# Kernel tuning notes

Measured on AMD Instinct MI355X. Metric: run time of the kernel, lower is better.

## Reference

```python
import jax, jax.numpy as jnp
import numpy as np

HIDDEN = 768
HEADS = 8
EXP = 4
EPS = 1e-5


def layer_norm(x, g, b):
    mu = jnp.mean(x, axis=-1, keepdims=True)
    var = jnp.mean(jnp.square(x - mu), axis=-1, keepdims=True)
    return (x - mu) * jax.lax.rsqrt(var + EPS) * g + b


def setup_inputs() -> dict:
    key = jax.random.key(0)
    ks = jax.random.split(key, 16)
    h, e = HIDDEN, EXP * HIDDEN
    s = 0.02
    return {
        "x": jax.random.normal(ks[0], (2, 4096, h), dtype=jnp.float32),
        "ln1_g": jnp.ones((h,), jnp.float32),
        "ln1_b": jnp.zeros((h,), jnp.float32),
        "wq": jax.random.normal(ks[1], (h, h), jnp.float32) * s,
        "bq": jnp.zeros((h,), jnp.float32),
        "wk": jax.random.normal(ks[2], (h, h), jnp.float32) * s,
        "bk": jnp.zeros((h,), jnp.float32),
        "wv": jax.random.normal(ks[3], (h, h), jnp.float32) * s,
        "bv": jnp.zeros((h,), jnp.float32),
        "wp": jax.random.normal(ks[4], (h, h), jnp.float32) * s,
        "bp": jnp.zeros((h,), jnp.float32),
        "ln2_g": jnp.ones((h,), jnp.float32),
        "ln2_b": jnp.zeros((h,), jnp.float32),
        "w1": jax.random.normal(ks[5], (h, e), jnp.float32) * s,
        "b1": jnp.zeros((e,), jnp.float32),
        "w2": jax.random.normal(ks[6], (e, h), jnp.float32) * s,
        "b2": jnp.zeros((h,), jnp.float32),
    }


def reference(x, ln1_g, ln1_b, wq, bq, wk, bk, wv, bv, wp, bp,
              ln2_g, ln2_b, w1, b1, w2, b2):
    n, s, h = x.shape
    d = h // HEADS

    # --- MSA branch (pre-LN) ---
    xn = layer_norm(x, ln1_g, ln1_b)
    q = (xn @ wq + bq).reshape(n, s, HEADS, d).transpose(0, 2, 1, 3)  # bhsd
    k = (xn @ wk + bk).reshape(n, s, HEADS, d).transpose(0, 2, 1, 3)
    v = (xn @ wv + bv).reshape(n, s, HEADS, d).transpose(0, 2, 1, 3)
    energy = jnp.einsum('bhqd,bhkd->bhqk', q, k)
    # faithful to original: softmax over the HEAD axis (dim=1), then scale
    att = jax.nn.softmax(energy, axis=1) / (h ** 0.5)
    attn_out = jnp.einsum('bhqk,bhkd->bhqd', att, v)
    attn_out = attn_out.transpose(0, 2, 1, 3).reshape(n, s, h)
    attn_out = attn_out @ wp + bp
    x = x + attn_out

    # --- MLP branch (pre-LN) ---
    xn = layer_norm(x, ln2_g, ln2_b)
    hmid = jax.nn.gelu(xn @ w1 + b1, approximate=False)
    x = x + (hmid @ w2 + b2)
    return x
```

## Files before the change

### kernel.cpp

```cpp
#include <hip/hip_runtime.h>
#include <cstdint>
#include <cstddef>

#define AS1 __attribute__((address_space(1)))
#define AS3 __attribute__((address_space(3)))

typedef __attribute__((ext_vector_type(8))) __bf16 bf16x8;
typedef __attribute__((ext_vector_type(4))) float f32x4;

__device__ __forceinline__ void gload_lds16(const void* g, void* l) {
  __builtin_amdgcn_global_load_lds((AS1 void*)g, (AS3 void*)l, 16, 0, 0);
}

__global__ void k_transpose_w(const float* __restrict__ src, __bf16* __restrict__ dst,
                              int K, int N, int ldd, int koff) {
  __shared__ float tile[32][33];
  const int bx = blockIdx.x * 32;
  const int by = blockIdx.y * 32;
  const int tx = threadIdx.x, ty = threadIdx.y;
#pragma unroll
  for (int ii = 0; ii < 4; ++ii) {
    int i = ty + ii * 8;
    tile[i][tx] = src[(size_t)(by + i) * N + bx + tx];
  }
  __syncthreads();
#pragma unroll
  for (int ii = 0; ii < 4; ++ii) {
    int i = ty + ii * 8;
    dst[(size_t)(bx + i) * ldd + koff + by + tx] = (__bf16)tile[tx][i];
  }
}

__global__ void k_transpose_w4(const float* __restrict__ s0, const float* __restrict__ s1,
                               const float* __restrict__ s2, const float* __restrict__ s3,
                               __bf16* __restrict__ d0, __bf16* __restrict__ d1,
                               __bf16* __restrict__ d2, __bf16* __restrict__ d3) {
  __shared__ float tile[32][33];
  const float* src;
  __bf16* dst;
  switch (blockIdx.z) {
    case 0: src = s0; dst = d0; break;
    case 1: src = s1; dst = d1; break;
    case 2: src = s2; dst = d2; break;
    default: src = s3; dst = d3; break;
  }
  const int bx = blockIdx.x * 32, by = blockIdx.y * 32;
  const int tx = threadIdx.x, ty = threadIdx.y;
#pragma unroll
  for (int ii = 0; ii < 4; ++ii) {
    int i = ty + ii * 8;
    tile[i][tx] = src[(size_t)(by + i) * 768 + bx + tx];
  }
  __syncthreads();
#pragma unroll
  for (int ii = 0; ii < 4; ++ii) {
    int i = ty + ii * 8;
    dst[(size_t)(bx + i) * 768 + by + tx] = (__bf16)tile[tx][i];
  }
}

__global__ void k_pack_bias(const float* __restrict__ bq, const float* __restrict__ bk,
                            const float* __restrict__ bv, float* __restrict__ dst) {
  int i = blockIdx.x * 256 + threadIdx.x;
  if (i < 768) dst[i] = bq[i];
  else if (i < 1536) dst[i] = bk[i - 768];
  else if (i < 2304) dst[i] = bv[i - 1536];
}

__global__ __launch_bounds__(256) void k_layernorm(const float* __restrict__ x,
                                                   const float* __restrict__ g,
                                                   const float* __restrict__ b,
                                                   __bf16* __restrict__ out) {
  const int row = blockIdx.x * 4 + (threadIdx.x >> 6);
  const int lane = threadIdx.x & 63;
  const float* xr = x + (size_t)row * 768;
  float4 v[3];
#pragma unroll
  for (int j = 0; j < 3; ++j) v[j] = *(const float4*)(xr + j * 256 + lane * 4);
  float s = 0.f, ss = 0.f;
#pragma unroll
  for (int j = 0; j < 3; ++j) {
    s += v[j].x + v[j].y + v[j].z + v[j].w;
    ss += v[j].x * v[j].x + v[j].y * v[j].y + v[j].z * v[j].z + v[j].w * v[j].w;
  }
#pragma unroll
  for (int off = 32; off > 0; off >>= 1) {
    s += __shfl_xor(s, off);
    ss += __shfl_xor(ss, off);
  }
  const float mu = s * (1.f / 768.f);
  const float rstd = rsqrtf(ss * (1.f / 768.f) - mu * mu + 1e-5f);
  __bf16* orow = out + (size_t)row * 768;
#pragma unroll
  for (int j = 0; j < 3; ++j) {
    float4 gg = *(const float4*)(g + j * 256 + lane * 4);
    float4 bb = *(const float4*)(b + j * 256 + lane * 4);
    const int base = j * 256 + lane * 4;
    orow[base + 0] = (__bf16)((v[j].x - mu) * rstd * gg.x + bb.x);
    orow[base + 1] = (__bf16)((v[j].y - mu) * rstd * gg.y + bb.y);
    orow[base + 2] = (__bf16)((v[j].z - mu) * rstd * gg.z + bb.z);
    orow[base + 3] = (__bf16)((v[j].w - mu) * rstd * gg.w + bb.w);
  }
}

template <int MODE>
__global__ __launch_bounds__(256) void k_gemm(const __bf16* __restrict__ A,
                                              const __bf16* __restrict__ BT,
                                              const float* __restrict__ bias,
                                              const float* __restrict__ resid,
                                              void* __restrict__ Cout,
                                              int M, int N, int K, int lda, int ldb) {
  __shared__ __bf16 As[128 * 32];
  __shared__ __bf16 Bs[128 * 32];
  const int nx = N >> 7;
  const int rpx = (M >> 7) >> 3;
  const int xcd = blockIdx.x & 7;
  const int ib = blockIdx.x >> 3;
  const int n0 = (ib % nx) << 7;
  const int m0 = (xcd * rpx + ib / nx) << 7;
  if constexpr (MODE == 3) {
    A += (size_t)blockIdx.y * K;
    BT += (size_t)blockIdx.y * K;
  }
  const int tid = threadIdx.x;
  const int wid = tid >> 6, lane = tid & 63;
  const int wm = wid >> 1, wn = wid & 1;
  const int lr = lane & 15, lg = lane >> 4;

  f32x4 acc[4][4] = {};

  for (int k0 = 0; k0 < K; k0 += 32) {
#pragma unroll
    for (int it = 0; it < 2; ++it) {
      int t = tid + it * 256;
      int r = t >> 2, c = (t & 3) * 8;
      gload_lds16(A + (size_t)(m0 + r) * lda + k0 + c, As + t * 8);
      gload_lds16(BT + (size_t)(n0 + r) * ldb + k0 + c, Bs + t * 8);
    }
    __syncthreads();
    bf16x8 af[4], bf[4];
#pragma unroll
    for (int i = 0; i < 4; ++i) af[i] = *(const bf16x8*)(As + (wm * 64 + i * 16 + lr) * 32 + lg * 8);
#pragma unroll
    for (int j = 0; j < 4; ++j) bf[j] = *(const bf16x8*)(Bs + (wn * 64 + j * 16 + lr) * 32 + lg * 8);
#pragma unroll
    for (int i = 0; i < 4; ++i)
#pragma unroll
      for (int j = 0; j < 4; ++j)
        acc[i][j] = __builtin_amdgcn_mfma_f32_16x16x32_bf16(af[i], bf[j], acc[i][j], 0, 0, 0);
    __syncthreads();
  }

#pragma unroll
  for (int i = 0; i < 4; ++i)
#pragma unroll
    for (int j = 0; j < 4; ++j)
#pragma unroll
      for (int r = 0; r < 4; ++r) {
        int row = m0 + wm * 64 + i * 16 + lg * 4 + r;
        int col = n0 + wn * 64 + j * 16 + lr;
        float v = acc[i][j][r];
        if constexpr (MODE != 3) v += bias[col];
        size_t idx = (size_t)row * N + col;
        if constexpr (MODE == 0) {
          if (col < 768) v *= 1.44269504088896f;
          ((__bf16*)Cout)[idx] = (__bf16)v;
        } else if constexpr (MODE == 1) {
          ((float*)Cout)[idx] = v + resid[idx];
        } else if constexpr (MODE == 2) {
          float u = 0.7978845608f * (v + 0.044715f * v * v * v);
          float t = __builtin_amdgcn_exp2f(u * 2.88539008f);
          float th = 1.f - 2.f * __builtin_amdgcn_rcpf(t + 1.f);
          ((__bf16*)Cout)[idx] = (__bf16)(0.5f * v * (1.f + th));
        } else {
          ((__bf16*)Cout)[(size_t)blockIdx.y * M * N + idx] = (__bf16)v;
        }
      }
}

__global__ __launch_bounds__(256) void k_fuse_mlp2(const __bf16* __restrict__ p0,
                                                   const __bf16* __restrict__ p1,
                                                   const float* __restrict__ bias,
                                                   const float* __restrict__ resid,
                                                   float* __restrict__ out) {
  int g = blockIdx.x * 256 + threadIdx.x;
  int base = g * 8;
  int col = base % 768;
  bf16x8 a = *(const bf16x8*)(p0 + base);
  bf16x8 b = *(const bf16x8*)(p1 + base);
  float4 r0 = *(const float4*)(resid + base);
  float4 r1 = *(const float4*)(resid + base + 4);
  float4 b0 = *(const float4*)(bias + col);
  float4 b1 = *(const float4*)(bias + col + 4);
  float4 o0, o1;
  o0.x = r0.x + b0.x + (float)a[0] + (float)b[0];
  o0.y = r0.y + b0.y + (float)a[1] + (float)b[1];
  o0.z = r0.z + b0.z + (float)a[2] + (float)b[2];
  o0.w = r0.w + b0.w + (float)a[3] + (float)b[3];
  o1.x = r1.x + b1.x + (float)a[4] + (float)b[4];
  o1.y = r1.y + b1.y + (float)a[5] + (float)b[5];
  o1.z = r1.z + b1.z + (float)a[6] + (float)b[6];
  o1.w = r1.w + b1.w + (float)a[7] + (float)b[7];
  *(float4*)(out + base) = o0;
  *(float4*)(out + base + 4) = o1;
}

__global__ __launch_bounds__(256) void k_pack_kv(const __bf16* __restrict__ qkv,
                                                 __bf16* __restrict__ KA,
                                                 __bf16* __restrict__ VA) {
  __shared__ __bf16 vtile[32][772];
  const int g = blockIdx.x, b = blockIdx.y;
  const int t = threadIdx.x;
#pragma unroll
  for (int half = 0; half < 2; ++half) {
    int kb = g * 2 + half;
#pragma unroll
    for (int i = 0; i < 6; ++i) {
      int c = t + i * 256;
      int lane = c & 63, f = c >> 6;
      int dc = f % 3, hh = (f / 3) & 1, hp = f / 6;
      int row = kb * 16 + (lane & 15);
      int col = 768 + hp * 192 + hh * 96 + dc * 32 + (lane >> 4) * 8;
      bf16x8 v = *(const bf16x8*)(qkv + (size_t)(b * 4096 + row) * 2304 + col);
      *(bf16x8*)(KA + ((size_t)(b * 256 + kb) * 1536 + c) * 8) = v;
    }
  }
#pragma unroll
  for (int i = 0; i < 12; ++i) {
    int c = t + i * 256;
    int row = c / 96, c8 = c % 96;
    *(bf16x8*)(&vtile[row][c8 * 8]) =
        *(const bf16x8*)(qkv + (size_t)(b * 4096 + g * 32 + row) * 2304 + 1536 + c8 * 8);
  }
  __syncthreads();
#pragma unroll
  for (int i = 0; i < 12; ++i) {
    int c = t + i * 256;
    int lane = c & 63, f = c >> 6;
    int db = f % 6, hh = (f / 6) & 1, hp = f / 12;
    int d = hp * 192 + hh * 96 + db * 16 + (lane & 15);
    int lg_ = lane >> 4;
    bf16x8 v;
#pragma unroll
    for (int e = 0; e < 8; ++e) {
      int krow = (e >> 2) * 16 + lg_ * 4 + (e & 3);
      v[e] = vtile[krow][d];
    }
    *(bf16x8*)(VA + ((size_t)(b * 128 + g) * 3072 + c) * 8) = v;
  }
}

__global__ __launch_bounds__(1024, 4) void k_attn(const __bf16* __restrict__ qkv,
                                                  const __bf16* __restrict__ KA,
                                                  const __bf16* __restrict__ VA,
                                                  __bf16* __restrict__ attn2) {
  __shared__ __bf16 Kb_s[2][12288];
  __shared__ __bf16 Vb_s[24576];
  __shared__ float ps_s[2][4352];
  const int bid = blockIdx.x;
  const int slice = bid & 3;
  const int b = slice >> 1, ks = slice & 1;
  const int qb = bid >> 2;
  const int wid = threadIdx.x >> 6;
  const int qs = wid & 3, hp = wid >> 2;
  const int q0 = qb * 64 + qs * 16;
  const int lane = threadIdx.x & 63;
  const int lr = lane & 15, lg = lane >> 4;

  const __bf16* Qb = qkv + (size_t)(b * 4096 + q0) * 2304;
  bf16x8 qf[2][3];
#pragma unroll
  for (int hh = 0; hh < 2; ++hh)
#pragma unroll
    for (int dc = 0; dc < 3; ++dc)
      qf[hh][dc] = *(const bf16x8*)(Qb + (size_t)lr * 2304 + (hp * 2 + hh) * 96 + dc * 32 + lg * 8);

  const int L1 = wid, hpK1 = L1 / 6, jK1 = L1 - hpK1 * 6;
  const int L2 = wid + 16, hpK2 = L2 / 6, jK2 = L2 - hpK2 * 6;

  int kb = ks * 128;
  {
    const __bf16* srcK = KA + (size_t)(b * 256 + kb) * 12288;
    gload_lds16(srcK + hpK1 * 3072 + jK1 * 512 + lane * 8,
                &Kb_s[0][hpK1 * 3072 + jK1 * 512 + lane * 8]);
    if (wid < 8)
      gload_lds16(srcK + hpK2 * 3072 + jK2 * 512 + lane * 8,
                  &Kb_s[0][hpK2 * 3072 + jK2 * 512 + lane * 8]);
  }
  asm volatile("s_waitcnt vmcnt(0)" ::: "memory");
  __builtin_amdgcn_s_barrier();
  asm volatile("" ::: "memory");

  f32x4 o[2][6] = {};
  f32x4 eA[2], eB[2];

#define HALF(ET, PAR, DO_V, DO_PV) do {                                               \
    {                      \
      size_t kidx = (size_t)(b * 256 + kb + 1);                                       \
      size_t kmax = (size_t)(b * 256 + 255);                                          \
      if (kidx > kmax) kidx = kmax;                                                   \
      const __bf16* srcK = KA + kidx * 12288;                                         \
      gload_lds16(srcK + hpK1 * 3072 + jK1 * 512 + lane * 8,                          \
                  &Kb_s[PAR ^ 1][hpK1 * 3072 + jK1 * 512 + lane * 8]);                \
      if (wid < 8)                                                                    \
        gload_lds16(srcK + hpK2 * 3072 + jK2 * 512 + lane * 8,                        \
                    &Kb_s[PAR ^ 1][hpK2 * 3072 + jK2 * 512 + lane * 8]);              \
    }                                                                                 \
    if (DO_V) {     \
      const __bf16* srcV = VA + (size_t)(b * 128 + (kb >> 1)) * 24576;                \
      _Pragma("unroll")                                                               \
      for (int tt = 0; tt < 3; ++tt) {                                                \
        int L = wid * 3 + tt;                                                         \
        int hpV = L / 12, jV = L - hpV * 12;                                          \
        gload_lds16(srcV + hpV * 6144 + jV * 512 + lane * 8,                          \
                    &Vb_s[hpV * 6144 + jV * 512 + lane * 8]);                         \
      }                                                                               \
    }                                                                                 \
    ET[0] = (f32x4){0.f, 0.f, 0.f, 0.f};                                              \
    ET[1] = (f32x4){0.f, 0.f, 0.f, 0.f};                                              \
    {                                                                                 \
      const __bf16* kbase = &Kb_s[PAR][hp * 3072 + lane * 8];                         \
      __builtin_amdgcn_s_setprio(1);                                                  \
      _Pragma("unroll")                                                               \
      for (int hh = 0; hh < 2; ++hh)                                                  \
        _Pragma("unroll")                                                             \
        for (int dc = 0; dc < 3; ++dc) {                                              \
          bf16x8 kf = *(const bf16x8*)(kbase + (hh * 3 + dc) * 512);                  \
          ET[hh] = __builtin_amdgcn_mfma_f32_16x16x32_bf16(kf, qf[hh][dc], ET[hh],    \
                                                           0, 0, 0);                  \
        }                                                                             \
      __builtin_amdgcn_s_setprio(0);                                                  \
    }                                                                                 \
    _Pragma("unroll")                                                                 \
    for (int rr = 0; rr < 4; ++rr) {                                                  \
      float e0 = __builtin_amdgcn_exp2f(ET[0][rr]);                                   \
      float e1 = __builtin_amdgcn_exp2f(ET[1][rr]);                                   \
      ET[0][rr] = e0;                                                                 \
      ET[1][rr] = e1;                                                                 \
      ps_s[PAR][qs * 1088 + (lg * 4 + rr) * 68 + hp * 17 + lr] = e0 + e1;             \
    }                                                                                 \
    if (DO_V) {                                                                       \
      asm volatile("s_waitcnt vmcnt(3) lgkmcnt(0)" ::: "memory");                     \
    } else {                                                                          \
      asm volatile("s_waitcnt vmcnt(0) lgkmcnt(0)" ::: "memory");                     \
    }                                                                                 \
    __builtin_amdgcn_s_barrier();                                                     \
    asm volatile("" ::: "memory");                                                    \
    {                                                                                 \
      float inv_[4];                                                                  \
      _Pragma("unroll")                                                               \
      for (int rr = 0; rr < 4; ++rr) {                                                \
        const int base = qs * 1088 + (lg * 4 + rr) * 68 + lr;                         \
        float tot = (ps_s[PAR][base] + ps_s[PAR][base + 17]) +                        \
                    (ps_s[PAR][base + 34] + ps_s[PAR][base + 51]);                    \
        inv_[rr] = 0.03608439182435161f * __builtin_amdgcn_rcpf(tot);                 \
      }                                                                               \
      _Pragma("unroll")                                                               \
      for (int rr = 0; rr < 4; ++rr) {                                                \
        ET[0][rr] *= inv_[rr];                                                        \
        ET[1][rr] *= inv_[rr];                                                        \
      }                                                                               \
    }                                                                                 \
    if (DO_PV) {                                                                      \
      bf16x8 pf0, pf1;                                                                \
      _Pragma("unroll")                                                               \
      for (int e2 = 0; e2 < 8; ++e2) {                                                \
        int rr = e2 & 3;                                                              \
        if (e2 < 4) { pf0[e2] = (__bf16)eA[0][rr]; pf1[e2] = (__bf16)eA[1][rr]; }     \
        else        { pf0[e2] = (__bf16)eB[0][rr]; pf1[e2] = (__bf16)eB[1][rr]; }     \
      }                                                                               \
      const __bf16* vbase = &Vb_s[hp * 6144 + lane * 8];                              \
      __builtin_amdgcn_s_setprio(1);                                                  \
      _Pragma("unroll")                                                               \
      for (int db = 0; db < 6; ++db) {                                                \
        bf16x8 vf0 = *(const bf16x8*)(vbase + db * 512);                              \
        bf16x8 vf1 = *(const bf16x8*)(vbase + (6 + db) * 512);                        \
        o[0][db] = __builtin_amdgcn_mfma_f32_16x16x32_bf16(pf0, vf0, o[0][db], 0, 0, 0); \
        o[1][db] = __builtin_amdgcn_mfma_f32_16x16x32_bf16(pf1, vf1, o[1][db], 0, 0, 0); \
      }                                                                               \
      __builtin_amdgcn_s_setprio(0);                                                  \
    }                                                                                 \
    ++kb;                                                                             \
  } while (0)

  for (int rp = 0; rp < 128; rp += 2) {
    HALF(eA, 0, 1, 0);
    HALF(eB, 1, 0, 1);
  }
#undef HALF

#pragma unroll
  for (int hh = 0; hh < 2; ++hh)
#pragma unroll
    for (int db = 0; db < 6; ++db)
#pragma unroll
      for (int rr = 0; rr < 4; ++rr)
        attn2[(size_t)(b * 4096 + q0 + lg * 4 + rr) * 1536 + ks * 768 +
              (hp * 2 + hh) * 96 + db * 16 + lr] = (__bf16)o[hh][db][rr];
}

__global__ __launch_bounds__(256) void k_reduce_attn(const __bf16* __restrict__ attn2,
                                                     __bf16* __restrict__ out) {
  int g = blockIdx.x * 256 + threadIdx.x;
  int row = g / 96, c8 = g % 96;
  const __bf16* p = attn2 + (size_t)row * 1536 + c8 * 8;
  bf16x8 v0 = *(const bf16x8*)(p);
  bf16x8 v1 = *(const bf16x8*)(p + 768);
  bf16x8 r;
#pragma unroll
  for (int e = 0; e < 8; ++e) r[e] = (__bf16)((float)v0[e] + (float)v1[e]);
  *(bf16x8*)(out + (size_t)row * 768 + c8 * 8) = r;
}

extern "C" void kernel_launch(void* const* d_in, const int* in_sizes, int n_in,
                              void* d_out, int out_size, void* d_ws, size_t ws_size,
                              hipStream_t stream) {
  (void)in_sizes; (void)n_in; (void)out_size; (void)ws_size;
  const float* x     = (const float*)d_in[0];
  const float* ln1_g = (const float*)d_in[1];
  const float* ln1_b = (const float*)d_in[2];
  const float* wq    = (const float*)d_in[3];
  const float* bq    = (const float*)d_in[4];
  const float* wk    = (const float*)d_in[5];
  const float* bk    = (const float*)d_in[6];
  const float* wv    = (const float*)d_in[7];
  const float* bv    = (const float*)d_in[8];
  const float* wp    = (const float*)d_in[9];
  const float* bp    = (const float*)d_in[10];
  const float* ln2_g = (const float*)d_in[11];
  const float* ln2_b = (const float*)d_in[12];
  const float* w1    = (const float*)d_in[13];
  const float* b1    = (const float*)d_in[14];
  const float* w2    = (const float*)d_in[15];
  const float* b2    = (const float*)d_in[16];

  char* ws = (char*)d_ws;
  const size_t o_wqkvT = 0;
  const size_t o_wpT   = o_wqkvT + (size_t)2304 * 768 * 2;
  const size_t o_w1T   = o_wpT   + (size_t)768 * 768 * 2;
  const size_t o_w2T   = o_w1T   + (size_t)768 * 3072 * 2;
  const size_t o_bqkv  = o_w2T   + (size_t)3072 * 768 * 2;
  const size_t o_xn    = o_bqkv  + (size_t)2304 * 4;
  const size_t o_qkv   = o_xn    + (size_t)8192 * 768 * 2;
  const size_t o_KA    = o_qkv   + (size_t)8192 * 2304 * 2;
  const size_t o_VA    = o_KA    + (size_t)2 * 256 * 1536 * 8 * 2;
  const size_t o_attn2 = o_VA    + (size_t)2 * 128 * 3072 * 8 * 2;
  const size_t o_x1      = o_attn2;
  const size_t o_part    = o_attn2 + (size_t)8192 * 768 * 4;
  const size_t o_attnred = o_KA;
  const size_t o_xn2     = o_VA;
  const size_t o_hmid    = o_xn;

  __bf16* wqkvT = (__bf16*)(ws + o_wqkvT);
  __bf16* wpT   = (__bf16*)(ws + o_wpT);
  __bf16* w1T   = (__bf16*)(ws + o_w1T);
  __bf16* w2T   = (__bf16*)(ws + o_w2T);
  float*  bqkv  = (float*)(ws + o_bqkv);
  __bf16* xn    = (__bf16*)(ws + o_xn);
  __bf16* qkvb  = (__bf16*)(ws + o_qkv);
  __bf16* KA    = (__bf16*)(ws + o_KA);
  __bf16* VA    = (__bf16*)(ws + o_VA);
  __bf16* attn2 = (__bf16*)(ws + o_attn2);
  float*  x1    = (float*)(ws + o_x1);
  __bf16* part  = (__bf16*)(ws + o_part);
  __bf16* attnr = (__bf16*)(ws + o_attnred);
  __bf16* xn2   = (__bf16*)(ws + o_xn2);
  __bf16* hmid  = (__bf16*)(ws + o_hmid);

  dim3 tb(32, 8);
  k_transpose_w4<<<dim3(24, 24, 4), tb, 0, stream>>>(wq, wk, wv, wp,
                                                     wqkvT, wqkvT + (size_t)768 * 768,
                                                     wqkvT + (size_t)2 * 768 * 768, wpT);
  k_transpose_w<<<dim3(96, 24), tb, 0, stream>>>(w1, w1T, 768, 3072, 768, 0);
  k_transpose_w<<<dim3(24, 96), tb, 0, stream>>>(w2, w2T, 3072, 768, 3072, 0);
  k_pack_bias<<<9, 256, 0, stream>>>(bq, bk, bv, bqkv);

  k_layernorm<<<2048, 256, 0, stream>>>(x, ln1_g, ln1_b, xn);
  k_gemm<0><<<1152, 256, 0, stream>>>(xn, wqkvT, bqkv, nullptr, qkvb, 8192, 2304, 768, 768, 768);
  k_pack_kv<<<dim3(128, 2), 256, 0, stream>>>(qkvb, KA, VA);
  k_attn<<<256, 1024, 0, stream>>>(qkvb, KA, VA, attn2);
  k_reduce_attn<<<3072, 256, 0, stream>>>(attn2, attnr);
  k_gemm<1><<<384, 256, 0, stream>>>(attnr, wpT, bp, x, x1, 8192, 768, 768, 768, 768);
  k_layernorm<<<2048, 256, 0, stream>>>(x1, ln2_g, ln2_b, xn2);
  k_gemm<2><<<1536, 256, 0, stream>>>(xn2, w1T, b1, nullptr, hmid, 8192, 3072, 768, 768, 768);
  k_gemm<3><<<dim3(384, 2), 256, 0, stream>>>(hmid, w2T, nullptr, nullptr, part,
                                              8192, 768, 1536, 3072, 3072);
  k_fuse_mlp2<<<3072, 256, 0, stream>>>(part, part + (size_t)8192 * 768, b2, x1,
                                        (float*)d_out);
}
```

Baseline: 445.9 us.

## Merge prep kernels into one launch and store residual x1 in bf16

Folds the weight transposes, bias packing and first layernorm into a single k_prep launch that dispatches on block index, removing several kernel launches. It also stores the post-attention residual x1 as bf16 instead of fp32, so the second layernorm and the final residual add read half the bytes. The trade-off is lower precision in the residual stream, and k_prep now uses a branch-heavy grid with mixed work per block.

Result: faster. 435.6 us, median of 2 (-2.3%).

```diff
diff --git a/kernel.cpp b/kernel.cpp
--- a/kernel.cpp
+++ b/kernel.cpp
@@ -6,82 +6,131 @@
 #define AS3 __attribute__((address_space(3)))
 
 typedef __attribute__((ext_vector_type(8))) __bf16 bf16x8;
+typedef __attribute__((ext_vector_type(4))) __bf16 bf16x4;
 typedef __attribute__((ext_vector_type(4))) float f32x4;
 
 __device__ __forceinline__ void gload_lds16(const void* g, void* l) {
   __builtin_amdgcn_global_load_lds((AS1 void*)g, (AS3 void*)l, 16, 0, 0);
 }
 
-__global__ void k_transpose_w(const float* __restrict__ src, __bf16* __restrict__ dst,
-                              int K, int N, int ldd, int koff) {
+__global__ __launch_bounds__(256) void k_prep(
+    const float* __restrict__ wq, const float* __restrict__ wk,
+    const float* __restrict__ wv, const float* __restrict__ wp,
+    const float* __restrict__ w1, const float* __restrict__ w2,
+    const float* __restrict__ bq, const float* __restrict__ bk,
+    const float* __restrict__ bv,
+    const float* __restrict__ x, const float* __restrict__ ln1_g,
+    const float* __restrict__ ln1_b,
+    __bf16* __restrict__ wqkvT, __bf16* __restrict__ wpT,
+    __bf16* __restrict__ w1T, __bf16* __restrict__ w2T,
+    float* __restrict__ bqkv, __bf16* __restrict__ xn) {
   __shared__ float tile[32][33];
-  const int bx = blockIdx.x * 32;
-  const int by = blockIdx.y * 32;
-  const int tx = threadIdx.x, ty = threadIdx.y;
-#pragma unroll
-  for (int ii = 0; ii < 4; ++ii) {
-    int i = ty + ii * 8;
-    tile[i][tx] = src[(size_t)(by + i) * N + bx + tx];
-  }
-  __syncthreads();
-#pragma unroll
-  for (int ii = 0; ii < 4; ++ii) {
-    int i = ty + ii * 8;
-    dst[(size_t)(bx + i) * ldd + koff + by + tx] = (__bf16)tile[tx][i];
-  }
-}
-
-__global__ void k_transpose_w4(const float* __restrict__ s0, const float* __restrict__ s1,
-                               const float* __restrict__ s2, const float* __restrict__ s3,
-                               __bf16* __restrict__ d0, __bf16* __restrict__ d1,
-                               __bf16* __restrict__ d2, __bf16* __restrict__ d3) {
-  __shared__ float tile[32][33];
-  const float* src;
-  __bf16* dst;
-  switch (blockIdx.z) {
-    case 0: src = s0; dst = d0; break;
-    case 1: src = s1; dst = d1; break;
-    case 2: src = s2; dst = d2; break;
-    default: src = s3; dst = d3; break;
-  }
-  const int bx = blockIdx.x * 32, by = blockIdx.y * 32;
-  const int tx = threadIdx.x, ty = threadIdx.y;
-#pragma unroll
-  for (int ii = 0; ii < 4; ++ii) {
-    int i = ty + ii * 8;
-    tile[i][tx] = src[(size_t)(by + i) * 768 + bx + tx];
-  }
-  __syncthreads();
-#pragma unroll
-  for (int ii = 0; ii < 4; ++ii) {
-    int i = ty + ii * 8;
-    dst[(size_t)(bx + i) * 768 + by + tx] = (__bf16)tile[tx][i];
-  }
-}
-
-__global__ void k_pack_bias(const float* __restrict__ bq, const float* __restrict__ bk,
-                            const float* __restrict__ bv, float* __restrict__ dst) {
-  int i = blockIdx.x * 256 + threadIdx.x;
-  if (i < 768) dst[i] = bq[i];
-  else if (i < 1536) dst[i] = bk[i - 768];
-  else if (i < 2304) dst[i] = bv[i - 1536];
-}
-
-__global__ __launch_bounds__(256) void k_layernorm(const float* __restrict__ x,
-                                                   const float* __restrict__ g,
-                                                   const float* __restrict__ b,
-                                                   __bf16* __restrict__ out) {
+  const int bid = blockIdx.x;
+  const int t = threadIdx.x;
+  const int tx = t & 31, ty = t >> 5;
+
+  if (bid < 2304) {
+    const int which = bid / 576, r = bid % 576;
+    const float* src = which == 0 ? wq : which == 1 ? wk : which == 2 ? wv : wp;
+    __bf16* dst = which == 3 ? wpT : wqkvT + (size_t)which * 768 * 768;
+    const int bx = (r % 24) * 32, by = (r / 24) * 32;
+#pragma unroll
+    for (int ii = 0; ii < 4; ++ii) {
+      int i = ty + ii * 8;
+      tile[i][tx] = src[(size_t)(by + i) * 768 + bx + tx];
+    }
+    __syncthreads();
+#pragma unroll
+    for (int ii = 0; ii < 4; ++ii) {
+      int i = ty + ii * 8;
+      dst[(size_t)(bx + i) * 768 + by + tx] = (__bf16)tile[tx][i];
+    }
+  } else if (bid < 4608) {
+    const int r = bid - 2304;
+    const int bx = (r % 96) * 32, by = (r / 96) * 32;
+#pragma unroll
+    for (int ii = 0; ii < 4; ++ii) {
+      int i = ty + ii * 8;
+      tile[i][tx] = w1[(size_t)(by + i) * 3072 + bx + tx];
+    }
+    __syncthreads();
+#pragma unroll
+    for (int ii = 0; ii < 4; ++ii) {
+      int i = ty + ii * 8;
+      w1T[(size_t)(bx + i) * 768 + by + tx] = (__bf16)tile[tx][i];
+    }
+  } else if (bid < 6912) {
+    const int r = bid - 4608;
+    const int bx = (r % 24) * 32, by = (r / 24) * 32;
+#pragma unroll
+    for (int ii = 0; ii < 4; ++ii) {
+      int i = ty + ii * 8;
+      tile[i][tx] = w2[(size_t)(by + i) * 768 + bx + tx];
+    }
+    __syncthreads();
+#pragma unroll
+    for (int ii = 0; ii < 4; ++ii) {
+      int i = ty + ii * 8;
+      w2T[(size_t)(bx + i) * 3072 + by + tx] = (__bf16)tile[tx][i];
+    }
+  } else if (bid < 6921) {
+    int i = (bid - 6912) * 256 + t;
+    if (i < 768) bqkv[i] = bq[i];
+    else if (i < 1536) bqkv[i] = bk[i - 768];
+    else if (i < 2304) bqkv[i] = bv[i - 1536];
+  } else {
+    const int row = (bid - 6921) * 4 + (t >> 6);
+    const int lane = t & 63;
+    const float* xr = x + (size_t)row * 768;
+    float4 v[3];
+#pragma unroll
+    for (int j = 0; j < 3; ++j) v[j] = *(const float4*)(xr + j * 256 + lane * 4);
+    float s = 0.f, ss = 0.f;
+#pragma unroll
+    for (int j = 0; j < 3; ++j) {
+      s += v[j].x + v[j].y + v[j].z + v[j].w;
+      ss += v[j].x * v[j].x + v[j].y * v[j].y + v[j].z * v[j].z + v[j].w * v[j].w;
+    }
+#pragma unroll
+    for (int off = 32; off > 0; off >>= 1) {
+      s += __shfl_xor(s, off);
+      ss += __shfl_xor(ss, off);
+    }
+    const float mu = s * (1.f / 768.f);
+    const float rstd = rsqrtf(ss * (1.f / 768.f) - mu * mu + 1e-5f);
+    __bf16* orow = xn + (size_t)row * 768;
+#pragma unroll
+    for (int j = 0; j < 3; ++j) {
+      float4 gg = *(const float4*)(ln1_g + j * 256 + lane * 4);
+      float4 bb = *(const float4*)(ln1_b + j * 256 + lane * 4);
+      const int base = j * 256 + lane * 4;
+      orow[base + 0] = (__bf16)((v[j].x - mu) * rstd * gg.x + bb.x);
+      orow[base + 1] = (__bf16)((v[j].y - mu) * rstd * gg.y + bb.y);
+      orow[base + 2] = (__bf16)((v[j].z - mu) * rstd * gg.z + bb.z);
+      orow[base + 3] = (__bf16)((v[j].w - mu) * rstd * gg.w + bb.w);
+    }
+  }
+}
+
+__global__ __launch_bounds__(256) void k_layernorm_b(const __bf16* __restrict__ x,
+                                                     const float* __restrict__ g,
+                                                     const float* __restrict__ b,
+                                                     __bf16* __restrict__ out) {
   const int row = blockIdx.x * 4 + (threadIdx.x >> 6);
   const int lane = threadIdx.x & 63;
-  const float* xr = x + (size_t)row * 768;
-  float4 v[3];
-#pragma unroll
-  for (int j = 0; j < 3; ++j) v[j] = *(const float4*)(xr + j * 256 + lane * 4);
+  const __bf16* xr = x + (size_t)row * 768;
+  float v[12];
+#pragma unroll
+  for (int j = 0; j < 3; ++j) {
+    bf16x4 u = *(const bf16x4*)(xr + j * 256 + lane * 4);
+#pragma unroll
+    for (int e = 0; e < 4; ++e) v[j * 4 + e] = (float)u[e];
+  }
   float s = 0.f, ss = 0.f;
 #pragma unroll
-  for (int j = 0; j < 3; ++j) {
-    s += v[j].x + v[j].y + v[j].z + v[j].w;
-    ss += v[j].x * v[j].x + v[j].y * v[j].y + v[j].z * v[j].z + v[j].w * v[j].w;
+  for (int j = 0; j < 12; ++j) {
+    s += v[j];
+    ss += v[j] * v[j];
   }
 #pragma unroll
   for (int off = 32; off > 0; off >>= 1) {
@@ -96,10 +145,10 @@
     float4 gg = *(const float4*)(g + j * 256 + lane * 4);
     float4 bb = *(const float4*)(b + j * 256 + lane * 4);
     const int base = j * 256 + lane * 4;
-    orow[base + 0] = (__bf16)((v[j].x - mu) * rstd * gg.x + bb.x);
-    orow[base + 1] = (__bf16)((v[j].y - mu) * rstd * gg.y + bb.y);
-    orow[base + 2] = (__bf16)((v[j].z - mu) * rstd * gg.z + bb.z);
-    orow[base + 3] = (__bf16)((v[j].w - mu) * rstd * gg.w + bb.w);
+    orow[base + 0] = (__bf16)((v[j * 4 + 0] - mu) * rstd * gg.x + bb.x);
+    orow[base + 1] = (__bf16)((v[j * 4 + 1] - mu) * rstd * gg.y + bb.y);
+    orow[base + 2] = (__bf16)((v[j * 4 + 2] - mu) * rstd * gg.z + bb.z);
+    orow[base + 3] = (__bf16)((v[j * 4 + 3] - mu) * rstd * gg.w + bb.w);
   }
 }
 
@@ -166,7 +215,7 @@
           if (col < 768) v *= 1.44269504088896f;
           ((__bf16*)Cout)[idx] = (__bf16)v;
         } else if constexpr (MODE == 1) {
-          ((float*)Cout)[idx] = v + resid[idx];
+          ((__bf16*)Cout)[idx] = (__bf16)(v + resid[idx]);
         } else if constexpr (MODE == 2) {
           float u = 0.7978845608f * (v + 0.044715f * v * v * v);
           float t = __builtin_amdgcn_exp2f(u * 2.88539008f);
@@ -181,26 +230,25 @@
 __global__ __launch_bounds__(256) void k_fuse_mlp2(const __bf16* __restrict__ p0,
                                                    const __bf16* __restrict__ p1,
                                                    const float* __restrict__ bias,
-                                                   const float* __restrict__ resid,
+                                                   const __bf16* __restrict__ resid,
                                                    float* __restrict__ out) {
   int g = blockIdx.x * 256 + threadIdx.x;
   int base = g * 8;
   int col = base % 768;
   bf16x8 a = *(const bf16x8*)(p0 + base);
   bf16x8 b = *(const bf16x8*)(p1 + base);
-  float4 r0 = *(const float4*)(resid + base);
-  float4 r1 = *(const float4*)(resid + base + 4);
+  bf16x8 rr = *(const bf16x8*)(resid + base);
   float4 b0 = *(const float4*)(bias + col);
   float4 b1 = *(const float4*)(bias + col + 4);
   float4 o0, o1;
-  o0.x = r0.x + b0.x + (float)a[0] + (float)b[0];
-  o0.y = r0.y + b0.y + (float)a[1] + (float)b[1];
-  o0.z = r0.z + b0.z + (float)a[2] + (float)b[2];
-  o0.w = r0.w + b0.w + (float)a[3] + (float)b[3];
-  o1.x = r1.x + b1.x + (float)a[4] + (float)b[4];
-  o1.y = r1.y + b1.y + (float)a[5] + (float)b[5];
-  o1.z = r1.z + b1.z + (float)a[6] + (float)b[6];
-  o1.w = r1.w + b1.w + (float)a[7] + (float)b[7];
+  o0.x = (float)rr[0] + b0.x + (float)a[0] + (float)b[0];
+  o0.y = (float)rr[1] + b0.y + (float)a[1] + (float)b[1];
+  o0.z = (float)rr[2] + b0.z + (float)a[2] + (float)b[2];
+  o0.w = (float)rr[3] + b0.w + (float)a[3] + (float)b[3];
+  o1.x = (float)rr[4] + b1.x + (float)a[4] + (float)b[4];
+  o1.y = (float)rr[5] + b1.y + (float)a[5] + (float)b[5];
+  o1.z = (float)rr[6] + b1.z + (float)a[6] + (float)b[6];
+  o1.w = (float)rr[7] + b1.w + (float)a[7] + (float)b[7];
   *(float4*)(out + base) = o0;
   *(float4*)(out + base + 4) = o1;
 }
@@ -461,30 +509,24 @@
   __bf16* KA    = (__bf16*)(ws + o_KA);
   __bf16* VA    = (__bf16*)(ws + o_VA);
   __bf16* attn2 = (__bf16*)(ws + o_attn2);
-  float*  x1    = (float*)(ws + o_x1);
+  __bf16* x1b   = (__bf16*)(ws + o_x1);
   __bf16* part  = (__bf16*)(ws + o_part);
   __bf16* attnr = (__bf16*)(ws + o_attnred);
   __bf16* xn2   = (__bf16*)(ws + o_xn2);
   __bf16* hmid  = (__bf16*)(ws + o_hmid);
 
-  dim3 tb(32, 8);
-  k_transpose_w4<<<dim3(24, 24, 4), tb, 0, stream>>>(wq, wk, wv, wp,
-                                                     wqkvT, wqkvT + (size_t)768 * 768,
-                                                     wqkvT + (size_t)2 * 768 * 768, wpT);
-  k_transpose_w<<<dim3(96, 24), tb, 0, stream>>>(w1, w1T, 768, 3072, 768, 0);
-  k_transpose_w<<<dim3(24, 96), tb, 0, stream>>>(w2, w2T, 3072, 768, 3072, 0);
-  k_pack_bias<<<9, 256, 0, stream>>>(bq, bk, bv, bqkv);
-
-  k_layernorm<<<2048, 256, 0, stream>>>(x, ln1_g, ln1_b, xn);
+  k_prep<<<8969, 256, 0, stream>>>(wq, wk, wv, wp, w1, w2, bq, bk, bv,
+                                   x, ln1_g, ln1_b,
+                                   wqkvT, wpT, w1T, w2T, bqkv, xn);
   k_gemm<0><<<1152, 256, 0, stream>>>(xn, wqkvT, bqkv, nullptr, qkvb, 8192, 2304, 768, 768, 768);
   k_pack_kv<<<dim3(128, 2), 256, 0, stream>>>(qkvb, KA, VA);
   k_attn<<<256, 1024, 0, stream>>>(qkvb, KA, VA, attn2);
   k_reduce_attn<<<3072, 256, 0, stream>>>(attn2, attnr);
-  k_gemm<1><<<384, 256, 0, stream>>>(attnr, wpT, bp, x, x1, 8192, 768, 768, 768, 768);
-  k_layernorm<<<2048, 256, 0, stream>>>(x1, ln2_g, ln2_b, xn2);
+  k_gemm<1><<<384, 256, 0, stream>>>(attnr, wpT, bp, x, x1b, 8192, 768, 768, 768, 768);
+  k_layernorm_b<<<2048, 256, 0, stream>>>(x1b, ln2_g, ln2_b, xn2);
   k_gemm<2><<<1536, 256, 0, stream>>>(xn2, w1T, b1, nullptr, hmid, 8192, 3072, 768, 768, 768);
   k_gemm<3><<<dim3(384, 2), 256, 0, stream>>>(hmid, w2T, nullptr, nullptr, part,
                                               8192, 768, 1536, 3072, 3072);
-  k_fuse_mlp2<<<3072, 256, 0, stream>>>(part, part + (size_t)8192 * 768, b2, x1,
+  k_fuse_mlp2<<<3072, 256, 0, stream>>>(part, part + (size_t)8192 * 768, b2, x1b,
                                         (float*)d_out);
 }
```
